# Kernel tuning notes

Hardware: AMD Instinct MI355X
Metric: run time of the kernel (lower is better)

The kernel has to match this reference:

```python
import jax, jax.numpy as jnp
import numpy as np

N, D_IN, D_OUT, E = 8192, 2048, 8192, 8


def setup_inputs() -> dict:
    key = jax.random.key(0)
    k1, k2, k3 = jax.random.split(key, 3)
    x = jax.random.normal(k1, (N, D_IN), dtype=jnp.float32)
    # packed weight layout [E, in, out] (pack() pretransposes [E,out,in] -> [E,in,out])
    weight = jax.random.normal(k2, (E, D_IN, D_OUT), dtype=jnp.float32) * (1.0 / np.sqrt(D_IN))
    indices = jax.random.randint(k3, (N,), 0, E, dtype=jnp.int32)
    return {"x": x, "weight": weight, "indices": indices}


def reference(x, weight, indices):
    # gather_mm: out[n] = x[n] @ weight[indices[n]]  -> [N, D_OUT]
    # Avoid materializing weight[indices] ([N, in, out]); instead loop over the
    # small fixed expert count, masking tokens routed to each expert.
    n_experts = weight.shape[0]
    out = jnp.zeros((x.shape[0], weight.shape[-1]), dtype=x.dtype)
    for e in range(n_experts):
        mask = (indices == e)[:, None]
        xe = jnp.where(mask, x, 0)          # zero out tokens not routed to e
        out = out + xe @ weight[e]           # [N, in] @ [in, out]
    return out
```

## Files before the change

### kernel.cpp

```cpp
#include <hip/hip_runtime.h>
#include <hip/hip_bf16.h>
#include <stdint.h>

#define N_TOK 8192
#define D_IN  2048
#define D_OUT 8192
#define NEXP  8
#define KST   32
#define NT2   40
#define NS2   32
#define AIMG  32768
#define X_OFF2 65536
#define X_BYTES2 ((long)NT2 * KST * AIMG)
#define W_OFF2 (X_OFF2 + X_BYTES2)
#define W_BYTES2 ((long)NEXP * NS2 * KST * AIMG)
#define WS_NEED2 ((size_t)(W_OFF2 + W_BYTES2))


typedef float  f32x4  __attribute__((ext_vector_type(4)));
typedef __bf16 bf16x8 __attribute__((ext_vector_type(8)));

__global__ void SwitchLinear_setup_kernel(const int* __restrict__ idx,
                                          int* __restrict__ ws) {
    __shared__ int cnt[NEXP], cur[NEXP];
    int t = threadIdx.x;
    if (t < NEXP) cnt[t] = 0;
    __syncthreads();
    for (int i = t; i < N_TOK; i += 256) atomicAdd(&cnt[idx[i]], 1);
    __syncthreads();
    if (t == 0) {
        int o = 0, nt = 0, nt1 = 0;
        for (int e = 0; e < NEXP; ++e) {
            cur[e] = o;
            int c = cnt[e];
            for (int r = 0; r < c; r += 256) {
                ws[8 + nt]   = e;
                ws[96 + nt]  = o + r;
                ws[192 + nt] = (c - r < 256) ? (c - r) : 256;
                ++nt;
            }
            for (int r = 0; r < c; r += 128) {
                ws[256 + nt1] = e;
                ws[328 + nt1] = o + r;
                ws[400 + nt1] = (c - r < 128) ? (c - r) : 128;
                ++nt1;
            }
            o += c;
        }
        ws[0] = nt;
        ws[4] = nt1;
    }
    __syncthreads();
    for (int i = t; i < N_TOK; i += 256) {
        int p = atomicAdd(&cur[idx[i]], 1);
        ws[512 + p] = i;
    }
}


__global__ __launch_bounds__(256) void SwitchLinear_convx_kernel(
    const float* __restrict__ x, const int* __restrict__ ws,
    char* __restrict__ wsb) {
    const int tile = blockIdx.x, kst = blockIdx.y;
    if (tile >= ws[0]) return;
    const int rs = ws[96 + tile], rows = ws[192 + tile];
    char* img = wsb + X_OFF2 + (long)(tile * KST + kst) * AIMG;
    const int t = threadIdx.x;
#pragma unroll
    for (int i = 0; i < 8; ++i) {
        int u = t + i * 256;
        int R = u >> 3, kc8 = u & 7;
        int rl = rs + (R < rows ? R : rows - 1);
        int token = ws[512 + rl];
        const float* src = x + (long)token * D_IN + kst * 64 + kc8 * 8;
        f32x4 v0 = *(const f32x4*)src;
        f32x4 v1 = *(const f32x4*)(src + 4);
        union { __bf16 hh[8]; uint4 u4; } c;
        c.hh[0] = (__bf16)v0[0]; c.hh[1] = (__bf16)v0[1];
        c.hh[2] = (__bf16)v0[2]; c.hh[3] = (__bf16)v0[3];
        c.hh[4] = (__bf16)v1[0]; c.hh[5] = (__bf16)v1[1];
        c.hh[6] = (__bf16)v1[2]; c.hh[7] = (__bf16)v1[3];
        int slot = (((R & 1) << 2) | (kc8 & 3)) ^ ((R >> 1) & 7);
        *(uint4*)(img + (kc8 >> 2) * 16384 + ((R >> 1) << 7) + (slot << 4)) = c.u4;
    }
}

__global__ __launch_bounds__(256) void SwitchLinear_convw_kernel(
    const float* __restrict__ w, char* __restrict__ wsb) {
    const int img = blockIdx.x;
    const int kst = img & 31, s = (img >> 5) & 63, e = img >> 11;
    const int y = s >> 1, hh = s & 1;
    __shared__ float tl[64 * 129];
    const float* src = w + (long)e * D_IN * D_OUT + (long)(kst * 64) * D_OUT +
                       y * 256 + hh * 128;
    const int t = threadIdx.x;
#pragma unroll
    for (int i = 0; i < 8; ++i) {
        int u = t + i * 256;
        int row = u >> 5, ch = u & 31;
        f32x4 v = *(const f32x4*)(src + (long)row * D_OUT + ch * 4);
        float* d = &tl[row * 129 + ch * 4];
        d[0] = v[0]; d[1] = v[1]; d[2] = v[2]; d[3] = v[3];
    }
    __syncthreads();
    char* dimg = wsb + W_OFF2 + (long)((e * NS2 + y) * KST + kst) * AIMG;
#pragma unroll
    for (int i = 0; i < 4; ++i) {
        int u = t + i * 256;
        int cl = u >> 3, kc8 = u & 7;
        union { __bf16 h8[8]; uint4 u4; } c;
#pragma unroll
        for (int j = 0; j < 8; ++j) c.h8[j] = (__bf16)tl[(kc8 * 8 + j) * 129 + cl];
        int cc = hh * 128 + cl;
        int slot = (((cc & 1) << 2) | (kc8 & 3)) ^ ((cc >> 1) & 7);
        *(uint4*)(dimg + (kc8 >> 2) * 16384 + ((cc >> 1) << 7) + (slot << 4)) = c.u4;
    }
}


__global__ __launch_bounds__(512, 1) void SwitchLinear_gemm_kernel(
    const char* __restrict__ wsb, const int* __restrict__ ws,
    float* __restrict__ out) {
    const int bid = blockIdx.x;
    const int lb  = (bid & 7) * ((NT2 * NS2) / 8) + (bid >> 3);
    const int tx  = lb % NT2;
    const int y   = lb / NT2;
    if (tx >= ws[0]) return;
    const int e = ws[8 + tx], rs = ws[96 + tx], rows = ws[192 + tx];

    __shared__ __align__(16) char lds[2][2][2][16384];
    __shared__ int ord[256];

    const int t = threadIdx.x;
    if (t < 256) ord[t] = ws[512 + rs + (t < rows ? t : 0)];
    __syncthreads();

    const char* aImg = wsb + X_OFF2 + (long)(tx * KST) * AIMG;
    const char* bImg = wsb + W_OFF2 + (long)((e * NS2 + y) * KST) * AIMG;

    const int lane = t & 63;
    const int wid  = t >> 6;
    const int wr = wid >> 2, wc = wid & 3;
    const int lm = lane & 15, lk = lane >> 4;

    f32x4 acc[8][4];
#pragma unroll
    for (int i = 0; i < 8; ++i)
#pragma unroll
        for (int j = 0; j < 4; ++j) acc[i][j] = (f32x4){0.f, 0.f, 0.f, 0.f};

    bf16x8 aa[4], bb[4];

#define STG(op, ks, half, tt)                                                 \
    __builtin_amdgcn_global_load_lds(                                         \
        (const __attribute__((address_space(1))) uint32_t*)(                  \
            ((op) ? bImg : aImg) + (long)(tt) * AIMG + (ks) * 16384 +         \
            (half) * 8192 + t * 16),                                          \
        (__attribute__((address_space(3))) uint32_t*)(                        \
            &lds[(tt) & 1][op][ks][(half) * 8192 + t * 16]),                  \
        16, 0, 0)

#define SWB(r) ((((r) >> 1) << 7) + (((((((r) & 1) << 2)) | lk) ^ (((r) >> 1) & 7)) << 4))

#define LDB(p, ks)                                                            \
    do { _Pragma("unroll")                                                    \
        for (int ni = 0; ni < 4; ++ni) {                                      \
            int cc = wc * 64 + ni * 16 + lm;                                  \
            bb[ni] = *(const bf16x8*)(&lds[p][1][ks][SWB(cc)]);               \
        } } while (0)

#define LDA(p, ks, mh)                                                        \
    do { _Pragma("unroll")                                                    \
        for (int q = 0; q < 4; ++q) {                                         \
            int rr = wr * 128 + (mh) * 64 + q * 16 + lm;                      \
            aa[q] = *(const bf16x8*)(&lds[p][0][ks][SWB(rr)]);                \
        } } while (0)

#define MFMA16(mh)                                                            \
    do { _Pragma("unroll")                                                    \
        for (int q = 0; q < 4; ++q)                                           \
            _Pragma("unroll")                                                 \
            for (int ni = 0; ni < 4; ++ni)                                    \
                acc[(mh) * 4 + q][ni] = __builtin_amdgcn_mfma_f32_16x16x32_bf16( \
                    aa[q], bb[ni], acc[(mh) * 4 + q][ni], 0, 0, 0);           \
    } while (0)

#define PH(p, ks, mh, DOB, ISSUE, WAITASM)                                    \
    do {                                                                      \
        if (DOB) LDB(p, ks);                                                  \
        LDA(p, ks, mh);                                                       \
        ISSUE;                                                                \
        WAITASM;                                                              \
        __builtin_amdgcn_s_barrier();                                         \
        asm volatile("s_waitcnt lgkmcnt(0)" ::: "memory");                    \
        __builtin_amdgcn_sched_barrier(0);                                    \
        __builtin_amdgcn_s_setprio(1);                                        \
        MFMA16(mh);                                                           \
        __builtin_amdgcn_s_setprio(0);                                        \
        __builtin_amdgcn_s_barrier();                                         \
    } while (0)

    STG(0, 0, 0, 0); STG(0, 0, 1, 0); STG(1, 0, 0, 0); STG(1, 0, 1, 0);
    STG(0, 1, 0, 0); STG(0, 1, 1, 0); STG(1, 1, 0, 0); STG(1, 1, 1, 0);
    asm volatile("s_waitcnt vmcnt(4)" ::: "memory");
    __builtin_amdgcn_s_barrier();

    for (int tt = 0; tt < KST - 1; ++tt) {
        const int p = tt & 1;
        const int nx = tt + 1;
        PH(p, 0, 0, 1, { STG(0, 0, 0, nx); STG(0, 0, 1, nx); }, ((void)0));
        PH(p, 0, 1, 0, { STG(1, 0, 0, nx); STG(1, 0, 1, nx); },
           asm volatile("s_waitcnt vmcnt(4)" ::: "memory"));
        PH(p, 1, 0, 1, { STG(0, 1, 0, nx); STG(0, 1, 1, nx); }, ((void)0));
        PH(p, 1, 1, 0, { STG(1, 1, 0, nx); STG(1, 1, 1, nx); },
           asm volatile("s_waitcnt vmcnt(4)" ::: "memory"));
    }
    {
        const int p = (KST - 1) & 1;
        PH(p, 0, 0, 1, ((void)0), ((void)0));
        PH(p, 0, 1, 0, ((void)0),
           asm volatile("s_waitcnt vmcnt(0)" ::: "memory"));
        PH(p, 1, 0, 1, ((void)0), ((void)0));
        PH(p, 1, 1, 0, ((void)0), ((void)0));
    }

#pragma unroll
    for (int mi = 0; mi < 8; ++mi) {
#pragma unroll
        for (int j = 0; j < 4; ++j) {
            int rl = wr * 128 + mi * 16 + lk * 4 + j;
            if (rl < rows) {
                int token = ord[rl];
                float* po = out + (long)token * D_OUT + y * 256 + wc * 64 + lm;
#pragma unroll
                for (int ni = 0; ni < 4; ++ni) po[ni * 16] = acc[mi][ni][j];
            }
        }
    }
#undef STG
#undef SWB
#undef LDB
#undef LDA
#undef MFMA16
#undef PH
}


__device__ __forceinline__ int fb_a_byte(int r, int kbyte) {
    return r * 128 + (kbyte ^ ((r & 7) << 4));
}
__device__ __forceinline__ int fb_b_byte(int n, int kbyte) {
    int slot = (n ^ (n >> 2)) & 7;
    return n * 128 + (kbyte ^ (slot << 4));
}

__global__ __launch_bounds__(256, 2) void SwitchLinear_gemm_fb_kernel(
    const float* __restrict__ x, const float* __restrict__ w,
    const int* __restrict__ ws, float* __restrict__ out) {
    const int nt = ws[4];
    const int tx = blockIdx.x;
    if (tx >= nt) return;
    const int e    = ws[256 + tx];
    const int rs   = ws[328 + tx];
    const int rows = ws[400 + tx];
    const int col0 = blockIdx.y * 128;

    __shared__ __align__(16) unsigned short As[128 * 64];
    __shared__ __align__(16) unsigned short Bs[128 * 64];
    __shared__ int ord[128];

    const int t = threadIdx.x;
    if (t < 128) {
        int r = (t < rows) ? (rs + t) : rs;
        ord[t] = ws[512 + r];
    }
    __syncthreads();

    const int kq = t & 15;
    const float* pA[8];
    int rowA[8];
#pragma unroll
    for (int i = 0; i < 8; ++i) {
        int r = (t >> 4) + 16 * i;
        rowA[i] = r;
        pA[i] = x + (long)ord[r] * D_IN + kq * 4;
    }
    const float* pB[2];
    int nB[2], kbB[2];
#pragma unroll
    for (int i = 0; i < 2; ++i) {
        int u = t + 256 * i;
        int kg = u >> 5, q = u & 31;
        kbB[i] = kg * 4;
        nB[i]  = q * 4;
        pB[i]  = w + (long)e * D_IN * D_OUT + (long)(kg * 4) * D_OUT + col0 + q * 4;
    }

    const int lane = t & 63;
    const int wid  = t >> 6;
    const int wr = wid >> 1, wc = wid & 1;
    const int lm = lane & 15, lk = lane >> 4;

    f32x4 acc[4][4];
#pragma unroll
    for (int i = 0; i < 4; ++i)
#pragma unroll
        for (int j = 0; j < 4; ++j) acc[i][j] = (f32x4){0.f, 0.f, 0.f, 0.f};

    for (int k0 = 0; k0 < D_IN; k0 += 64) {
#pragma unroll
        for (int i = 0; i < 8; ++i) {
            f32x4 v = *(const f32x4*)(pA[i] + k0);
            union { __bf16 h[4]; uint2 u; } c;
            c.h[0] = (__bf16)v[0]; c.h[1] = (__bf16)v[1];
            c.h[2] = (__bf16)v[2]; c.h[3] = (__bf16)v[3];
            *(uint2*)((char*)As + fb_a_byte(rowA[i], kq * 8)) = c.u;
        }
#pragma unroll
        for (int i = 0; i < 2; ++i) {
            const float* p = pB[i] + (long)k0 * D_OUT;
            f32x4 r0 = *(const f32x4*)(p);
            f32x4 r1 = *(const f32x4*)(p + D_OUT);
            f32x4 r2 = *(const f32x4*)(p + 2 * D_OUT);
            f32x4 r3 = *(const f32x4*)(p + 3 * D_OUT);
#pragma unroll
            for (int j = 0; j < 4; ++j) {
                int n = nB[i] + j;
                union { __bf16 h[4]; uint2 u; } c;
                c.h[0] = (__bf16)r0[j]; c.h[1] = (__bf16)r1[j];
                c.h[2] = (__bf16)r2[j]; c.h[3] = (__bf16)r3[j];
                *(uint2*)((char*)Bs + fb_b_byte(n, kbB[i] * 2)) = c.u;
            }
        }
        __syncthreads();
#pragma unroll
        for (int ks = 0; ks < 2; ++ks) {
            bf16x8 a[4], b[4];
            const int kbyte = ks * 64 + lk * 16;
#pragma unroll
            for (int mi = 0; mi < 4; ++mi) {
                int r = wr * 64 + mi * 16 + lm;
                a[mi] = *(const bf16x8*)((const char*)As + fb_a_byte(r, kbyte));
            }
#pragma unroll
            for (int ni = 0; ni < 4; ++ni) {
                int n = wc * 64 + ni * 16 + lm;
                b[ni] = *(const bf16x8*)((const char*)Bs + fb_b_byte(n, kbyte));
            }
#pragma unroll
            for (int mi = 0; mi < 4; ++mi)
#pragma unroll
                for (int ni = 0; ni < 4; ++ni)
                    acc[mi][ni] = __builtin_amdgcn_mfma_f32_16x16x32_bf16(
                        a[mi], b[ni], acc[mi][ni], 0, 0, 0);
        }
        __syncthreads();
    }
#pragma unroll
    for (int mi = 0; mi < 4; ++mi) {
#pragma unroll
        for (int j = 0; j < 4; ++j) {
            int rl = wr * 64 + mi * 16 + lk * 4 + j;
            if (rl < rows) {
                int token = ord[rl];
                float* po = out + (long)token * D_OUT + col0 + wc * 64 + lm;
#pragma unroll
                for (int ni = 0; ni < 4; ++ni) po[ni * 16] = acc[mi][ni][j];
            }
        }
    }
}

extern "C" void kernel_launch(void* const* d_in, const int* in_sizes, int n_in,
                              void* d_out, int out_size, void* d_ws, size_t ws_size,
                              hipStream_t stream) {
    const float* x   = (const float*)d_in[0];
    const float* w   = (const float*)d_in[1];
    const int*   idx = (const int*)d_in[2];
    float* out = (float*)d_out;
    int*   ws  = (int*)d_ws;
    char*  wsb = (char*)d_ws;

    SwitchLinear_setup_kernel<<<1, 256, 0, stream>>>(idx, ws);
    if (ws_size >= WS_NEED2) {
        SwitchLinear_convx_kernel<<<dim3(NT2, KST), 256, 0, stream>>>(x, ws, wsb);
        SwitchLinear_convw_kernel<<<NEXP * 64 * KST, 256, 0, stream>>>(w, wsb);
        SwitchLinear_gemm_kernel<<<NT2 * NS2, 512, 0, stream>>>(wsb, ws, out);
    } else {
        dim3 grid(72, 64);
        SwitchLinear_gemm_fb_kernel<<<grid, 256, 0, stream>>>(x, w, ws, out);
    }
}
```

Before: 565.3 us.

## Fuse fp32 weight conversion into GEMM mainloop, drop separate convw pass

Removes the separate kernel that converted the full fp32 weight tensor into swizzled bf16 images in the workspace. The GEMM now loads fp32 weight tiles into registers, converts them to bf16 and writes them into a swizzled LDS layout inside the pipelined K loop. This avoids writing and re-reading the converted weights (about 128 MB) and one launch. In exchange each GEMM block does redundant conversion work on weights shared across token tiles, reads the larger fp32 data and uses more registers. The wait points are restructured to hide this work behind the MFMAs.

```diff
diff --git a/kernel.cpp b/kernel.cpp
--- a/kernel.cpp
+++ b/kernel.cpp
@@ -12,10 +12,7 @@
 #define AIMG  32768
 #define X_OFF2 65536
 #define X_BYTES2 ((long)NT2 * KST * AIMG)
-#define W_OFF2 (X_OFF2 + X_BYTES2)
-#define W_BYTES2 ((long)NEXP * NS2 * KST * AIMG)
-#define WS_NEED2 ((size_t)(W_OFF2 + W_BYTES2))
-
+#define WS_NEED2 ((size_t)(X_OFF2 + X_BYTES2))
 
 typedef float  f32x4  __attribute__((ext_vector_type(4)));
 typedef __bf16 bf16x8 __attribute__((ext_vector_type(8)));
@@ -85,42 +82,10 @@
     }
 }
 
-__global__ __launch_bounds__(256) void SwitchLinear_convw_kernel(
-    const float* __restrict__ w, char* __restrict__ wsb) {
-    const int img = blockIdx.x;
-    const int kst = img & 31, s = (img >> 5) & 63, e = img >> 11;
-    const int y = s >> 1, hh = s & 1;
-    __shared__ float tl[64 * 129];
-    const float* src = w + (long)e * D_IN * D_OUT + (long)(kst * 64) * D_OUT +
-                       y * 256 + hh * 128;
-    const int t = threadIdx.x;
-#pragma unroll
-    for (int i = 0; i < 8; ++i) {
-        int u = t + i * 256;
-        int row = u >> 5, ch = u & 31;
-        f32x4 v = *(const f32x4*)(src + (long)row * D_OUT + ch * 4);
-        float* d = &tl[row * 129 + ch * 4];
-        d[0] = v[0]; d[1] = v[1]; d[2] = v[2]; d[3] = v[3];
-    }
-    __syncthreads();
-    char* dimg = wsb + W_OFF2 + (long)((e * NS2 + y) * KST + kst) * AIMG;
-#pragma unroll
-    for (int i = 0; i < 4; ++i) {
-        int u = t + i * 256;
-        int cl = u >> 3, kc8 = u & 7;
-        union { __bf16 h8[8]; uint4 u4; } c;
-#pragma unroll
-        for (int j = 0; j < 8; ++j) c.h8[j] = (__bf16)tl[(kc8 * 8 + j) * 129 + cl];
-        int cc = hh * 128 + cl;
-        int slot = (((cc & 1) << 2) | (kc8 & 3)) ^ ((cc >> 1) & 7);
-        *(uint4*)(dimg + (kc8 >> 2) * 16384 + ((cc >> 1) << 7) + (slot << 4)) = c.u4;
-    }
-}
-
 
 __global__ __launch_bounds__(512, 1) void SwitchLinear_gemm_kernel(
-    const char* __restrict__ wsb, const int* __restrict__ ws,
-    float* __restrict__ out) {
+    const char* __restrict__ wsb, const float* __restrict__ w,
+    const int* __restrict__ ws, float* __restrict__ out) {
     const int bid = blockIdx.x;
     const int lb  = (bid & 7) * ((NT2 * NS2) / 8) + (bid >> 3);
     const int tx  = lb % NT2;
@@ -128,7 +93,8 @@
     if (tx >= ws[0]) return;
     const int e = ws[8 + tx], rs = ws[96 + tx], rows = ws[192 + tx];
 
-    __shared__ __align__(16) char lds[2][2][2][16384];
+    __shared__ __align__(16) char Asm[2][32768];
+    __shared__ __align__(16) char Bsm[2][32768];
     __shared__ int ord[256];
 
     const int t = threadIdx.x;
@@ -136,7 +102,9 @@
     __syncthreads();
 
     const char* aImg = wsb + X_OFF2 + (long)(tx * KST) * AIMG;
-    const char* bImg = wsb + W_OFF2 + (long)((e * NS2 + y) * KST) * AIMG;
+    const int kg = t & 7;
+    const int cg = t >> 3;
+    const float* bP = w + (long)e * D_IN * D_OUT + y * 256 + cg * 4;
 
     const int lane = t & 63;
     const int wid  = t >> 6;
@@ -150,30 +118,53 @@
         for (int j = 0; j < 4; ++j) acc[i][j] = (f32x4){0.f, 0.f, 0.f, 0.f};
 
     bf16x8 aa[4], bb[4];
-
-#define STG(op, ks, half, tt)                                                 \
+    f32x4 rB[2][4];
+
+#define STGA(ks, half, tt)                                                    \
     __builtin_amdgcn_global_load_lds(                                         \
         (const __attribute__((address_space(1))) uint32_t*)(                  \
-            ((op) ? bImg : aImg) + (long)(tt) * AIMG + (ks) * 16384 +         \
-            (half) * 8192 + t * 16),                                          \
+            aImg + (long)(tt) * AIMG + (ks) * 16384 + (half) * 8192 + t * 16),\
         (__attribute__((address_space(3))) uint32_t*)(                        \
-            &lds[(tt) & 1][op][ks][(half) * 8192 + t * 16]),                  \
+            &Asm[(tt) & 1][(ks) * 16384 + (half) * 8192 + t * 16]),           \
         16, 0, 0)
 
-#define SWB(r) ((((r) >> 1) << 7) + (((((((r) & 1) << 2)) | lk) ^ (((r) >> 1) & 7)) << 4))
+#define BLOAD(i, tt)                                                          \
+    do { _Pragma("unroll")                                                    \
+        for (int j = 0; j < 4; ++j)                                           \
+            rB[i][j] = *(const f32x4*)(bP +                                   \
+                (long)((tt) * 64 + (i) * 32 + kg * 4 + j) * D_OUT);           \
+    } while (0)
+
+#define CVTW(i, bp)                                                           \
+    do { char* bw = Bsm[bp] + (i) * 16384;                                    \
+        _Pragma("unroll")                                                     \
+        for (int j2 = 0; j2 < 4; ++j2) {                                      \
+            int cc = cg * 4 + j2;                                             \
+            int Xs = ((cc >> 1) ^ (cc >> 2)) & 7;                             \
+            int slot = ((((cc & 1) << 2)) | (kg >> 1)) ^ Xs;                  \
+            union { __bf16 h4[4]; uint2 u2; } c;                              \
+            c.h4[0] = (__bf16)rB[i][0][j2]; c.h4[1] = (__bf16)rB[i][1][j2];   \
+            c.h4[2] = (__bf16)rB[i][2][j2]; c.h4[3] = (__bf16)rB[i][3][j2];   \
+            *(uint2*)(bw + (cc >> 1) * 128 + slot * 16 + (kg & 1) * 8) = c.u2;\
+        } } while (0)
+
+#define SWA(r) (((r) >> 1) * 128 + ((((((r) & 1) << 2) | lk) ^ (((r) >> 1) & 7)) << 4))
+
+#define LDA(p, ks, mh)                                                        \
+    do { _Pragma("unroll")                                                    \
+        for (int q = 0; q < 4; ++q) {                                         \
+            int rr = wr * 128 + (mh) * 64 + q * 16 + lm;                      \
+            aa[q] = *(const bf16x8*)(&Asm[p][(ks) * 16384 + SWA(rr)]);        \
+        } } while (0)
 
 #define LDB(p, ks)                                                            \
     do { _Pragma("unroll")                                                    \
         for (int ni = 0; ni < 4; ++ni) {                                      \
             int cc = wc * 64 + ni * 16 + lm;                                  \
-            bb[ni] = *(const bf16x8*)(&lds[p][1][ks][SWB(cc)]);               \
-        } } while (0)
-
-#define LDA(p, ks, mh)                                                        \
-    do { _Pragma("unroll")                                                    \
-        for (int q = 0; q < 4; ++q) {                                         \
-            int rr = wr * 128 + (mh) * 64 + q * 16 + lm;                      \
-            aa[q] = *(const bf16x8*)(&lds[p][0][ks][SWB(rr)]);                \
+            int Xs = ((cc >> 1) ^ (cc >> 2)) & 7;                             \
+            int slot = ((((cc & 1) << 2)) | lk) ^ Xs;                         \
+            bb[ni] = *(const bf16x8*)(&Bsm[p][(ks) * 16384 +                  \
+                         (cc >> 1) * 128 + slot * 16]);                       \
         } } while (0)
 
 #define MFMA16(mh)                                                            \
@@ -185,41 +176,49 @@
                     aa[q], bb[ni], acc[(mh) * 4 + q][ni], 0, 0, 0);           \
     } while (0)
 
-#define PH(p, ks, mh, DOB, ISSUE, WAITASM)                                    \
+#define PH(p, ks, mh, DOB, ISSUE, POST)                                       \
     do {                                                                      \
         if (DOB) LDB(p, ks);                                                  \
         LDA(p, ks, mh);                                                       \
         ISSUE;                                                                \
-        WAITASM;                                                              \
         __builtin_amdgcn_s_barrier();                                         \
         asm volatile("s_waitcnt lgkmcnt(0)" ::: "memory");                    \
         __builtin_amdgcn_sched_barrier(0);                                    \
         __builtin_amdgcn_s_setprio(1);                                        \
         MFMA16(mh);                                                           \
         __builtin_amdgcn_s_setprio(0);                                        \
+        POST;                                                                 \
         __builtin_amdgcn_s_barrier();                                         \
     } while (0)
 
-    STG(0, 0, 0, 0); STG(0, 0, 1, 0); STG(1, 0, 0, 0); STG(1, 0, 1, 0);
-    STG(0, 1, 0, 0); STG(0, 1, 1, 0); STG(1, 1, 0, 0); STG(1, 1, 1, 0);
-    asm volatile("s_waitcnt vmcnt(4)" ::: "memory");
+    STGA(0, 0, 0); STGA(0, 1, 0); STGA(1, 0, 0); STGA(1, 1, 0);
+    BLOAD(0, 0); BLOAD(1, 0);
+    CVTW(0, 0); CVTW(1, 0);
+    asm volatile("s_waitcnt vmcnt(0)" ::: "memory");
+    asm volatile("s_waitcnt lgkmcnt(0)" ::: "memory");
     __builtin_amdgcn_s_barrier();
 
     for (int tt = 0; tt < KST - 1; ++tt) {
         const int p = tt & 1;
         const int nx = tt + 1;
-        PH(p, 0, 0, 1, { STG(0, 0, 0, nx); STG(0, 0, 1, nx); }, ((void)0));
-        PH(p, 0, 1, 0, { STG(1, 0, 0, nx); STG(1, 0, 1, nx); },
-           asm volatile("s_waitcnt vmcnt(4)" ::: "memory"));
-        PH(p, 1, 0, 1, { STG(0, 1, 0, nx); STG(0, 1, 1, nx); }, ((void)0));
-        PH(p, 1, 1, 0, { STG(1, 1, 0, nx); STG(1, 1, 1, nx); },
-           asm volatile("s_waitcnt vmcnt(4)" ::: "memory"));
+        PH(p, 0, 0, 1,
+           { STGA(0, 0, nx); STGA(0, 1, nx); BLOAD(0, nx); },
+           ((void)0));
+        PH(p, 0, 1, 0,
+           { STGA(1, 0, nx); STGA(1, 1, nx); BLOAD(1, nx); },
+           ((void)0));
+        PH(p, 1, 0, 1, ((void)0),
+           { CVTW(0, p ^ 1);
+             asm volatile("s_waitcnt lgkmcnt(0)" ::: "memory"); });
+        PH(p, 1, 1, 0, ((void)0),
+           { CVTW(1, p ^ 1);
+             asm volatile("s_waitcnt vmcnt(0)" ::: "memory");
+             asm volatile("s_waitcnt lgkmcnt(0)" ::: "memory"); });
     }
     {
         const int p = (KST - 1) & 1;
         PH(p, 0, 0, 1, ((void)0), ((void)0));
-        PH(p, 0, 1, 0, ((void)0),
-           asm volatile("s_waitcnt vmcnt(0)" ::: "memory"));
+        PH(p, 0, 1, 0, ((void)0), ((void)0));
         PH(p, 1, 0, 1, ((void)0), ((void)0));
         PH(p, 1, 1, 0, ((void)0), ((void)0));
     }
@@ -237,10 +236,12 @@
             }
         }
     }
-#undef STG
-#undef SWB
+#undef STGA
+#undef BLOAD
+#undef CVTW
+#undef SWA
+#undef LDA
 #undef LDB
-#undef LDA
 #undef MFMA16
 #undef PH
 }
@@ -290,10 +291,10 @@
 #pragma unroll
     for (int i = 0; i < 2; ++i) {
         int u = t + 256 * i;
-        int kg = u >> 5, q = u & 31;
-        kbB[i] = kg * 4;
+        int kgf = u >> 5, q = u & 31;
+        kbB[i] = kgf * 4;
         nB[i]  = q * 4;
-        pB[i]  = w + (long)e * D_IN * D_OUT + (long)(kg * 4) * D_OUT + col0 + q * 4;
+        pB[i]  = w + (long)e * D_IN * D_OUT + (long)(kgf * 4) * D_OUT + col0 + q * 4;
     }
 
     const int lane = t & 63;
@@ -384,8 +385,7 @@
     SwitchLinear_setup_kernel<<<1, 256, 0, stream>>>(idx, ws);
     if (ws_size >= WS_NEED2) {
         SwitchLinear_convx_kernel<<<dim3(NT2, KST), 256, 0, stream>>>(x, ws, wsb);
-        SwitchLinear_convw_kernel<<<NEXP * 64 * KST, 256, 0, stream>>>(w, wsb);
-        SwitchLinear_gemm_kernel<<<NT2 * NS2, 512, 0, stream>>>(wsb, ws, out);
+        SwitchLinear_gemm_kernel<<<NT2 * NS2, 512, 0, stream>>>(wsb, w, ws, out);
     } else {
         dim3 grid(72, 64);
         SwitchLinear_gemm_fb_kernel<<<grid, 256, 0, stream>>>(x, w, ws, out);
```

Measured after the change: 583.0 us. +3.1%, slower.
